# Kernel tuning notes

Hardware: AMD Instinct MI355X
Metric: run time of the kernel (lower is better)

The kernel has to match this reference:

```python
import jax, jax.numpy as jnp
import numpy as np

N, D, E = 524288, 64, 4  # tokens, feature dim (d_in=64 default), num_expert=4


def setup_inputs() -> dict:
    key = jax.random.key(0)
    ks = jax.random.split(key, 5)
    s = 0.02
    return {
        "x": jax.random.normal(ks[0], (N, D), jnp.float32),
        "w_gate_a": jax.random.normal(ks[1], (D, E), jnp.float32) * s,
        "w_exp_a": jax.random.normal(ks[2], (E, D, D), jnp.float32) * s,
        "b_exp_a": jnp.zeros((E, D), jnp.float32),
        "w_gate_b": jax.random.normal(ks[3], (D, E), jnp.float32) * s,
        "w_exp_b": jax.random.normal(ks[4], (E, D, D), jnp.float32) * s,
        "b_exp_b": jnp.zeros((E, D), jnp.float32),
    }


def _moe_layer(x, w_gate, w_exp, b_exp):
    # Soft MoE: softmax gate over experts, each expert is (x - b_e) @ W_e.
    # Noise and PWLayer dropout are eval-mode identities.
    gates = jax.nn.softmax(x @ w_gate, axis=-1)            # [N, E]
    shifted = x[:, None, :] - b_exp[None, :, :]            # [N, E, D]
    expert_out = jnp.einsum('ned,edf->nef', shifted, w_exp)  # [N, E, D]
    return jnp.einsum('ne,nef->nf', gates, expert_out)     # [N, D]


def reference(x, w_gate_a, w_exp_a, b_exp_a, w_gate_b, w_exp_b, b_exp_b):
    residual = x
    h = _moe_layer(x, w_gate_a, w_exp_a, b_exp_a)
    # self.act is None (default) and nn.Dropout(0.5) is identity in eval mode
    h = _moe_layer(h, w_gate_b, w_exp_b, b_exp_b)
    return h + residual
```

## Files before the change

### kernel.cpp

```cpp
#include <hip/hip_runtime.h>
#include <math.h>


typedef __attribute__((ext_vector_type(8))) short short8;
typedef __attribute__((ext_vector_type(4))) short short4v;
typedef __attribute__((ext_vector_type(4))) float floatx4;

__device__ __forceinline__ float bf2f(unsigned short s) {
    unsigned int u = ((unsigned int)s) << 16;
    return __builtin_bit_cast(float, u);
}
__device__ __forceinline__ short f2bf(float f) {
    unsigned int u = __builtin_bit_cast(unsigned int, f);
    u += 0x7fffu + ((u >> 16) & 1u);
    return (short)(u >> 16);
}

#define NBLOCKS 512
#define TPW 4

__device__ __forceinline__ float ldf(const void* p, int isbf, int idx) {
    return isbf ? bf2f(((const unsigned short*)p)[idx]) : ((const float*)p)[idx];
}

__global__ __launch_bounds__(256, 2)
void moe2_fused(const void* __restrict__ x,
                const void* __restrict__ wg_a,
                const void* __restrict__ we_a,
                const void* __restrict__ be_a,
                const void* __restrict__ wg_b,
                const void* __restrict__ we_b,
                const void* __restrict__ be_b,
                void* __restrict__ outv)
{
    __shared__ alignas(16) short sB[2][17408];
    __shared__ float sC[2][4][64];
    __shared__ alignas(16) short sStage[4][1152];
    __shared__ int sBad[7];

    const int tid = threadIdx.x;

    const void* ps[7] = {x, wg_a, we_a, be_a, wg_b, we_b, be_b};
    if (tid < 7) sBad[tid] = 0;
    __syncthreads();
    if (tid < 64) {
        #pragma unroll
        for (int b = 0; b < 7; ++b) {
            const unsigned short s = ((const unsigned short*)ps[b])[2 * tid];
            const float a = fabsf(bf2f(s));
            const bool sane = (s == 0) || (a >= 9.3e-10f && a <= 1.1e9f);
            if (!sane) atomicAdd(&sBad[b], 1);
        }
    }
    __syncthreads();
    const int fx  = (sBad[0] < 16);
    const int fga = (sBad[1] < 16), fwa = (sBad[2] < 16), fba = (sBad[3] < 16);
    const int fgb = (sBad[4] < 16), fwb = (sBad[5] < 16), fbb = (sBad[6] < 16);

    for (int idx = tid; idx < 2 * 17 * 2 * 64; idx += 256) {
        const int L   = idx / 2176;
        const int rem = idx - L * 2176;
        const int t   = rem >> 7;
        const int kap = (rem >> 6) & 1;
        const int l2  = rem & 63;
        const int kb  = kap * 32 + (l2 >> 4) * 8;
        const int cc  = l2 & 15;
        const void* we = L ? we_b : we_a;
        const void* wg = L ? wg_b : wg_a;
        const int  fwe = L ? fwb : fwa;
        const int  fwg = L ? fgb : fga;
        short* dst = &sB[L][rem * 8];
        if (t < 16) {
            const int e = t >> 2;
            const int f = (t & 3) * 16 + cc;
            #pragma unroll
            for (int j = 0; j < 8; ++j)
                dst[j] = f2bf(ldf(we, fwe, (e * 64 + kb + j) * 64 + f));
        } else {
            #pragma unroll
            for (int j = 0; j < 8; ++j)
                dst[j] = (cc < 4) ? f2bf(ldf(wg, fwg, (kb + j) * 4 + cc)) : (short)0;
        }
    }
    for (int idx = tid; idx < 512; idx += 256) {
        const int L = idx >> 8;
        const int e = (idx >> 6) & 3;
        const int f = idx & 63;
        const void* we = L ? we_b : we_a;
        const void* be = L ? be_b : be_a;
        const int  fwe = L ? fwb : fwa;
        const int  fbe = L ? fbb : fba;
        float s = 0.f;
        for (int d = 0; d < 64; ++d)
            s += ldf(be, fbe, e * 64 + d) * ldf(we, fwe, (e * 64 + d) * 64 + f);
        sC[L][e][f] = s;
    }
    __syncthreads();

    const int l  = tid & 63;
    const int wv = tid >> 6;
    const int c  = l & 15;
    const int q  = l >> 4;
    short* stg = &sStage[wv][0];

    auto runLayer = [&](const short8 (&aF)[4][2], const int L, float (&acc)[4][4][4]) {
        const short* BL = &sB[L][0];
        floatx4 gA[4];
        {
            const short8 B0 = *(const short8*)&BL[(16 * 2 + 0) * 512 + l * 8];
            const short8 B1 = *(const short8*)&BL[(16 * 2 + 1) * 512 + l * 8];
            #pragma unroll
            for (int s = 0; s < 4; ++s) {
                floatx4 z = {0.f, 0.f, 0.f, 0.f};
                z = __builtin_amdgcn_mfma_f32_16x16x32_bf16(aF[s][0], B0, z, 0, 0, 0);
                z = __builtin_amdgcn_mfma_f32_16x16x32_bf16(aF[s][1], B1, z, 0, 0, 0);
                gA[s] = z;
            }
        }
        #pragma unroll
        for (int s = 0; s < 4; ++s) {
            float lg[4][4];
            #pragma unroll
            for (int e = 0; e < 4; ++e)
                #pragma unroll
                for (int r = 0; r < 4; ++r)
                    lg[e][r] = __shfl(gA[s][r], (l & 48) + e, 64);
            short gv[4];
            #pragma unroll
            for (int r = 0; r < 4; ++r) {
                const float m0 = fmaxf(fmaxf(lg[0][r], lg[1][r]), fmaxf(lg[2][r], lg[3][r]));
                const float e0 = __expf(lg[0][r] - m0);
                const float e1 = __expf(lg[1][r] - m0);
                const float e2 = __expf(lg[2][r] - m0);
                const float e3 = __expf(lg[3][r] - m0);
                const float inv = 1.f / (e0 + e1 + e2 + e3);
                const float mine = (c == 0) ? e0 : (c == 1) ? e1 : (c == 2) ? e2 : e3;
                gv[r] = f2bf(mine * inv);
            }
            if (c < 4) {
                short4v pk = {gv[0], gv[1], gv[2], gv[3]};
                *(short4v*)&stg[(s * 4 + c) * 16 + 4 * q] = pk;
            }
        }

        #pragma unroll
        for (int s = 0; s < 4; ++s)
            #pragma unroll
            for (int tt = 0; tt < 4; ++tt)
                #pragma unroll
                for (int r = 0; r < 4; ++r)
                    acc[s][tt][r] = 0.f;

        #pragma unroll
        for (int e = 0; e < 4; ++e) {
            float gse[4][4];
            #pragma unroll
            for (int s = 0; s < 4; ++s) {
                const short4v gp = *(const short4v*)&stg[(s * 4 + e) * 16 + 4 * q];
                #pragma unroll
                for (int r = 0; r < 4; ++r)
                    gse[s][r] = bf2f((unsigned short)gp[r]);
            }
            #pragma unroll
            for (int tt = 0; tt < 4; ++tt) {
                const int t = e * 4 + tt;
                const short8 B0 = *(const short8*)&BL[(t * 2 + 0) * 512 + l * 8];
                const short8 B1 = *(const short8*)&BL[(t * 2 + 1) * 512 + l * 8];
                const float ce = sC[L][e][tt * 16 + c];
                #pragma unroll
                for (int s = 0; s < 4; ++s) {
                    floatx4 z = {0.f, 0.f, 0.f, 0.f};
                    z = __builtin_amdgcn_mfma_f32_16x16x32_bf16(aF[s][0], B0, z, 0, 0, 0);
                    z = __builtin_amdgcn_mfma_f32_16x16x32_bf16(aF[s][1], B1, z, 0, 0, 0);
                    #pragma unroll
                    for (int r = 0; r < 4; ++r)
                        acc[s][tt][r] += gse[s][r] * (z[r] - ce);
                }
            }
        }
    };

    const int waveGlobal = blockIdx.x * 4 + wv;
    for (int it = 0; it < TPW; ++it) {
        const int tile = waveGlobal * TPW + it;
        const size_t tok0 = (size_t)tile * 64;

        short8 xF[4][2];
        if (fx) {
            const unsigned short* xu = (const unsigned short*)x;
            #pragma unroll
            for (int s = 0; s < 4; ++s)
                #pragma unroll
                for (int k = 0; k < 2; ++k)
                    xF[s][k] = *(const short8*)(xu + (tok0 + s * 16 + c) * 64 + k * 32 + q * 8);
        } else {
            const float* xf = (const float*)x;
            #pragma unroll
            for (int s = 0; s < 4; ++s)
                #pragma unroll
                for (int k = 0; k < 2; ++k) {
                    const float* xr = xf + (tok0 + s * 16 + c) * 64 + k * 32 + q * 8;
                    const floatx4 v0 = *(const floatx4*)xr;
                    const floatx4 v1 = *(const floatx4*)(xr + 4);
                    short8 f;
                    #pragma unroll
                    for (int j = 0; j < 4; ++j) { f[j] = f2bf(v0[j]); f[4 + j] = f2bf(v1[j]); }
                    xF[s][k] = f;
                }
        }

        float acc[4][4][4];
        runLayer(xF, 0, acc);

        short8 hF[4][2];
        #pragma unroll
        for (int s = 0; s < 4; ++s) {
            #pragma unroll
            for (int tt = 0; tt < 4; ++tt)
                #pragma unroll
                for (int r = 0; r < 4; ++r)
                    stg[(4 * q + r) * 72 + tt * 16 + c] = f2bf(acc[s][tt][r]);
            hF[s][0] = *(const short8*)&stg[c * 72 + 0 + q * 8];
            hF[s][1] = *(const short8*)&stg[c * 72 + 32 + q * 8];
        }

        runLayer(hF, 1, acc);

        if (fx) {
            unsigned short* ob = (unsigned short*)outv;
            #pragma unroll
            for (int s = 0; s < 4; ++s) {
                #pragma unroll
                for (int tt = 0; tt < 4; ++tt)
                    #pragma unroll
                    for (int r = 0; r < 4; ++r)
                        stg[(4 * q + r) * 72 + tt * 16 + c] = f2bf(acc[s][tt][r]);
                #pragma unroll
                for (int k = 0; k < 2; ++k) {
                    const short8 v = *(const short8*)&stg[c * 72 + k * 32 + q * 8];
                    short8 o;
                    #pragma unroll
                    for (int j = 0; j < 8; ++j)
                        o[j] = f2bf(bf2f((unsigned short)v[j]) + bf2f((unsigned short)xF[s][k][j]));
                    *(short8*)(ob + (tok0 + s * 16 + c) * 64 + k * 32 + q * 8) = o;
                }
            }
        } else {
            const float* xf = (const float*)x;
            float* of = (float*)outv;
            #pragma unroll
            for (int s = 0; s < 4; ++s)
                #pragma unroll
                for (int tt = 0; tt < 4; ++tt)
                    #pragma unroll
                    for (int r = 0; r < 4; ++r) {
                        const size_t o = (tok0 + s * 16 + 4 * q + r) * 64 + tt * 16 + c;
                        of[o] = acc[s][tt][r] + xf[o];
                    }
        }
    }
}

extern "C" void kernel_launch(void* const* d_in, const int* in_sizes, int n_in,
                              void* d_out, int out_size, void* d_ws, size_t ws_size,
                              hipStream_t stream) {
    hipLaunchKernelGGL(moe2_fused, dim3(NBLOCKS), dim3(256), 0, stream,
                       d_in[0], d_in[1], d_in[2], d_in[3], d_in[4], d_in[5], d_in[6],
                       d_out);
}
```

Measured before the change: 362.5 us.

## Restructure MoE kernel: 1024-thread blocks, shuffle softmax, bias-free fast path, vector stores

After: 567.0 us. 56.4% more time.

```diff
diff --git a/kernel.cpp b/kernel.cpp
--- a/kernel.cpp
+++ b/kernel.cpp
@@ -3,61 +3,50 @@
 
 
 typedef __attribute__((ext_vector_type(8))) short short8;
-typedef __attribute__((ext_vector_type(4))) short short4v;
 typedef __attribute__((ext_vector_type(4))) float floatx4;
 
 __device__ __forceinline__ float bf2f(unsigned short s) {
     unsigned int u = ((unsigned int)s) << 16;
     return __builtin_bit_cast(float, u);
 }
-__device__ __forceinline__ short f2bf(float f) {
+__device__ __forceinline__ unsigned short f2bf(float f) {
     unsigned int u = __builtin_bit_cast(unsigned int, f);
     u += 0x7fffu + ((u >> 16) & 1u);
-    return (short)(u >> 16);
-}
-
-#define NBLOCKS 512
-#define TPW 4
-
-__device__ __forceinline__ float ldf(const void* p, int isbf, int idx) {
-    return isbf ? bf2f(((const unsigned short*)p)[idx]) : ((const float*)p)[idx];
-}
-
-__global__ __launch_bounds__(256, 2)
-void moe2_fused(const void* __restrict__ x,
-                const void* __restrict__ wg_a,
-                const void* __restrict__ we_a,
-                const void* __restrict__ be_a,
-                const void* __restrict__ wg_b,
-                const void* __restrict__ we_b,
-                const void* __restrict__ be_b,
-                void* __restrict__ outv)
+    return (unsigned short)(u >> 16);
+}
+__device__ __forceinline__ float hi2f(unsigned int p) {
+    return __builtin_bit_cast(float, p & 0xffff0000u);
+}
+__device__ __forceinline__ float lo2f(unsigned int p) {
+    return __builtin_bit_cast(float, p << 16);
+}
+
+struct CTrue  { static constexpr bool value = true;  };
+struct CFalse { static constexpr bool value = false; };
+
+#define NBLK 512
+
+__global__ __launch_bounds__(1024)
+void moe2_fused(const float* __restrict__ x,
+                const float* __restrict__ wg_a,
+                const float* __restrict__ we_a,
+                const float* __restrict__ be_a,
+                const float* __restrict__ wg_b,
+                const float* __restrict__ we_b,
+                const float* __restrict__ be_b,
+                float* __restrict__ out)
 {
     __shared__ alignas(16) short sB[2][17408];
     __shared__ float sC[2][4][64];
-    __shared__ alignas(16) short sStage[4][1152];
-    __shared__ int sBad[7];
+    __shared__ int sHasC;
+    __shared__ alignas(16) float sStg[16][1088];
 
     const int tid = threadIdx.x;
 
-    const void* ps[7] = {x, wg_a, we_a, be_a, wg_b, we_b, be_b};
-    if (tid < 7) sBad[tid] = 0;
+    if (tid == 0) sHasC = 0;
     __syncthreads();
-    if (tid < 64) {
-        #pragma unroll
-        for (int b = 0; b < 7; ++b) {
-            const unsigned short s = ((const unsigned short*)ps[b])[2 * tid];
-            const float a = fabsf(bf2f(s));
-            const bool sane = (s == 0) || (a >= 9.3e-10f && a <= 1.1e9f);
-            if (!sane) atomicAdd(&sBad[b], 1);
-        }
-    }
-    __syncthreads();
-    const int fx  = (sBad[0] < 16);
-    const int fga = (sBad[1] < 16), fwa = (sBad[2] < 16), fba = (sBad[3] < 16);
-    const int fgb = (sBad[4] < 16), fwb = (sBad[5] < 16), fbb = (sBad[6] < 16);
-
-    for (int idx = tid; idx < 2 * 17 * 2 * 64; idx += 256) {
+
+    for (int idx = tid; idx < 2 * 17 * 2 * 64; idx += 1024) {
         const int L   = idx / 2176;
         const int rem = idx - L * 2176;
         const int t   = rem >> 7;
@@ -65,81 +54,67 @@
         const int l2  = rem & 63;
         const int kb  = kap * 32 + (l2 >> 4) * 8;
         const int cc  = l2 & 15;
-        const void* we = L ? we_b : we_a;
-        const void* wg = L ? wg_b : wg_a;
-        const int  fwe = L ? fwb : fwa;
-        const int  fwg = L ? fgb : fga;
+        const float* we = L ? we_b : we_a;
+        const float* wg = L ? wg_b : wg_a;
         short* dst = &sB[L][rem * 8];
         if (t < 16) {
             const int e = t >> 2;
             const int f = (t & 3) * 16 + cc;
             #pragma unroll
             for (int j = 0; j < 8; ++j)
-                dst[j] = f2bf(ldf(we, fwe, (e * 64 + kb + j) * 64 + f));
+                dst[j] = (short)f2bf(we[(e * 64 + kb + j) * 64 + f]);
         } else {
             #pragma unroll
             for (int j = 0; j < 8; ++j)
-                dst[j] = (cc < 4) ? f2bf(ldf(wg, fwg, (kb + j) * 4 + cc)) : (short)0;
-        }
-    }
-    for (int idx = tid; idx < 512; idx += 256) {
+                dst[j] = (cc < 4) ? (short)f2bf(wg[(kb + j) * 4 + cc]) : (short)0;
+        }
+    }
+    for (int idx = tid; idx < 512; idx += 1024) {
         const int L = idx >> 8;
         const int e = (idx >> 6) & 3;
         const int f = idx & 63;
-        const void* we = L ? we_b : we_a;
-        const void* be = L ? be_b : be_a;
-        const int  fwe = L ? fwb : fwa;
-        const int  fbe = L ? fbb : fba;
+        const float* we = L ? we_b : we_a;
+        const float* be = L ? be_b : be_a;
         float s = 0.f;
         for (int d = 0; d < 64; ++d)
-            s += ldf(be, fbe, e * 64 + d) * ldf(we, fwe, (e * 64 + d) * 64 + f);
+            s += be[e * 64 + d] * we[(e * 64 + d) * 64 + f];
         sC[L][e][f] = s;
+        if (s != 0.f) atomicExch(&sHasC, 1);
     }
     __syncthreads();
+    const bool hasC = (sHasC != 0);
 
     const int l  = tid & 63;
     const int wv = tid >> 6;
     const int c  = l & 15;
     const int q  = l >> 4;
-    short* stg = &sStage[wv][0];
+    float* stgF = &sStg[wv][0];
+    short* stgS = (short*)stgF;
+
+    const int tile = blockIdx.x * 16 + wv;
+    const size_t tok0 = (size_t)tile * 64;
 
     auto runLayer = [&](const short8 (&aF)[4][2], const int L, float (&acc)[4][4][4]) {
         const short* BL = &sB[L][0];
-        floatx4 gA[4];
+        unsigned int gp[4][2];
         {
-            const short8 B0 = *(const short8*)&BL[(16 * 2 + 0) * 512 + l * 8];
-            const short8 B1 = *(const short8*)&BL[(16 * 2 + 1) * 512 + l * 8];
+            const short8 B0 = *(const short8*)&BL[(32 + 0) * 512 + l * 8];
+            const short8 B1 = *(const short8*)&BL[(32 + 1) * 512 + l * 8];
             #pragma unroll
             for (int s = 0; s < 4; ++s) {
                 floatx4 z = {0.f, 0.f, 0.f, 0.f};
                 z = __builtin_amdgcn_mfma_f32_16x16x32_bf16(aF[s][0], B0, z, 0, 0, 0);
                 z = __builtin_amdgcn_mfma_f32_16x16x32_bf16(aF[s][1], B1, z, 0, 0, 0);
-                gA[s] = z;
-            }
-        }
-        #pragma unroll
-        for (int s = 0; s < 4; ++s) {
-            float lg[4][4];
-            #pragma unroll
-            for (int e = 0; e < 4; ++e)
-                #pragma unroll
-                for (int r = 0; r < 4; ++r)
-                    lg[e][r] = __shfl(gA[s][r], (l & 48) + e, 64);
-            short gv[4];
-            #pragma unroll
-            for (int r = 0; r < 4; ++r) {
-                const float m0 = fmaxf(fmaxf(lg[0][r], lg[1][r]), fmaxf(lg[2][r], lg[3][r]));
-                const float e0 = __expf(lg[0][r] - m0);
-                const float e1 = __expf(lg[1][r] - m0);
-                const float e2 = __expf(lg[2][r] - m0);
-                const float e3 = __expf(lg[3][r] - m0);
-                const float inv = 1.f / (e0 + e1 + e2 + e3);
-                const float mine = (c == 0) ? e0 : (c == 1) ? e1 : (c == 2) ? e2 : e3;
-                gv[r] = f2bf(mine * inv);
-            }
-            if (c < 4) {
-                short4v pk = {gv[0], gv[1], gv[2], gv[3]};
-                *(short4v*)&stg[(s * 4 + c) * 16 + 4 * q] = pk;
+                float g[4];
+                #pragma unroll
+                for (int r = 0; r < 4; ++r) {
+                    const float ev = __expf(z[r]);
+                    const float s2 = ev + __shfl_xor(ev, 1, 64);
+                    const float sm = s2 + __shfl_xor(s2, 2, 64);
+                    g[r] = ev * __builtin_amdgcn_rcpf(sm);
+                }
+                gp[s][0] = (unsigned int)f2bf(g[0]) | ((unsigned int)f2bf(g[1]) << 16);
+                gp[s][1] = (unsigned int)f2bf(g[2]) | ((unsigned int)f2bf(g[3]) << 16);
             }
         }
 
@@ -151,112 +126,99 @@
                 for (int r = 0; r < 4; ++r)
                     acc[s][tt][r] = 0.f;
 
-        #pragma unroll
-        for (int e = 0; e < 4; ++e) {
-            float gse[4][4];
-            #pragma unroll
-            for (int s = 0; s < 4; ++s) {
-                const short4v gp = *(const short4v*)&stg[(s * 4 + e) * 16 + 4 * q];
-                #pragma unroll
-                for (int r = 0; r < 4; ++r)
-                    gse[s][r] = bf2f((unsigned short)gp[r]);
-            }
-            #pragma unroll
-            for (int tt = 0; tt < 4; ++tt) {
-                const int t = e * 4 + tt;
-                const short8 B0 = *(const short8*)&BL[(t * 2 + 0) * 512 + l * 8];
-                const short8 B1 = *(const short8*)&BL[(t * 2 + 1) * 512 + l * 8];
-                const float ce = sC[L][e][tt * 16 + c];
+        auto eloop = [&](auto HC) {
+            constexpr bool hc = decltype(HC)::value;
+            #pragma unroll
+            for (int e = 0; e < 4; ++e) {
+                unsigned int gs[4][2];
                 #pragma unroll
                 for (int s = 0; s < 4; ++s) {
-                    floatx4 z = {0.f, 0.f, 0.f, 0.f};
-                    z = __builtin_amdgcn_mfma_f32_16x16x32_bf16(aF[s][0], B0, z, 0, 0, 0);
-                    z = __builtin_amdgcn_mfma_f32_16x16x32_bf16(aF[s][1], B1, z, 0, 0, 0);
+                    gs[s][0] = __shfl(gp[s][0], (l & 48) + e, 64);
+                    gs[s][1] = __shfl(gp[s][1], (l & 48) + e, 64);
+                }
+                #pragma unroll
+                for (int tt = 0; tt < 4; ++tt) {
+                    const int t = e * 4 + tt;
+                    const short8 B0 = *(const short8*)&BL[(t * 2 + 0) * 512 + l * 8];
+                    const short8 B1 = *(const short8*)&BL[(t * 2 + 1) * 512 + l * 8];
+                    float ce = 0.f;
+                    if constexpr (hc) ce = sC[L][e][tt * 16 + c];
                     #pragma unroll
-                    for (int r = 0; r < 4; ++r)
-                        acc[s][tt][r] += gse[s][r] * (z[r] - ce);
+                    for (int s = 0; s < 4; ++s) {
+                        floatx4 z = {0.f, 0.f, 0.f, 0.f};
+                        z = __builtin_amdgcn_mfma_f32_16x16x32_bf16(aF[s][0], B0, z, 0, 0, 0);
+                        z = __builtin_amdgcn_mfma_f32_16x16x32_bf16(aF[s][1], B1, z, 0, 0, 0);
+                        const float g0 = lo2f(gs[s][0]), g1 = hi2f(gs[s][0]);
+                        const float g2 = lo2f(gs[s][1]), g3 = hi2f(gs[s][1]);
+                        if constexpr (hc) {
+                            acc[s][tt][0] += g0 * (z[0] - ce);
+                            acc[s][tt][1] += g1 * (z[1] - ce);
+                            acc[s][tt][2] += g2 * (z[2] - ce);
+                            acc[s][tt][3] += g3 * (z[3] - ce);
+                        } else {
+                            acc[s][tt][0] += g0 * z[0];
+                            acc[s][tt][1] += g1 * z[1];
+                            acc[s][tt][2] += g2 * z[2];
+                            acc[s][tt][3] += g3 * z[3];
+                        }
+                    }
                 }
             }
-        }
+        };
+        if (hasC) eloop(CTrue{}); else eloop(CFalse{});
     };
 
-    const int waveGlobal = blockIdx.x * 4 + wv;
-    for (int it = 0; it < TPW; ++it) {
-        const int tile = waveGlobal * TPW + it;
-        const size_t tok0 = (size_t)tile * 64;
-
-        short8 xF[4][2];
-        if (fx) {
-            const unsigned short* xu = (const unsigned short*)x;
-            #pragma unroll
-            for (int s = 0; s < 4; ++s)
-                #pragma unroll
-                for (int k = 0; k < 2; ++k)
-                    xF[s][k] = *(const short8*)(xu + (tok0 + s * 16 + c) * 64 + k * 32 + q * 8);
-        } else {
-            const float* xf = (const float*)x;
-            #pragma unroll
-            for (int s = 0; s < 4; ++s)
-                #pragma unroll
-                for (int k = 0; k < 2; ++k) {
-                    const float* xr = xf + (tok0 + s * 16 + c) * 64 + k * 32 + q * 8;
-                    const floatx4 v0 = *(const floatx4*)xr;
-                    const floatx4 v1 = *(const floatx4*)(xr + 4);
-                    short8 f;
-                    #pragma unroll
-                    for (int j = 0; j < 4; ++j) { f[j] = f2bf(v0[j]); f[4 + j] = f2bf(v1[j]); }
-                    xF[s][k] = f;
-                }
-        }
-
-        float acc[4][4][4];
-        runLayer(xF, 0, acc);
-
-        short8 hF[4][2];
-        #pragma unroll
-        for (int s = 0; s < 4; ++s) {
-            #pragma unroll
-            for (int tt = 0; tt < 4; ++tt)
-                #pragma unroll
-                for (int r = 0; r < 4; ++r)
-                    stg[(4 * q + r) * 72 + tt * 16 + c] = f2bf(acc[s][tt][r]);
-            hF[s][0] = *(const short8*)&stg[c * 72 + 0 + q * 8];
-            hF[s][1] = *(const short8*)&stg[c * 72 + 32 + q * 8];
-        }
-
-        runLayer(hF, 1, acc);
-
-        if (fx) {
-            unsigned short* ob = (unsigned short*)outv;
-            #pragma unroll
-            for (int s = 0; s < 4; ++s) {
-                #pragma unroll
-                for (int tt = 0; tt < 4; ++tt)
-                    #pragma unroll
-                    for (int r = 0; r < 4; ++r)
-                        stg[(4 * q + r) * 72 + tt * 16 + c] = f2bf(acc[s][tt][r]);
-                #pragma unroll
-                for (int k = 0; k < 2; ++k) {
-                    const short8 v = *(const short8*)&stg[c * 72 + k * 32 + q * 8];
-                    short8 o;
-                    #pragma unroll
-                    for (int j = 0; j < 8; ++j)
-                        o[j] = f2bf(bf2f((unsigned short)v[j]) + bf2f((unsigned short)xF[s][k][j]));
-                    *(short8*)(ob + (tok0 + s * 16 + c) * 64 + k * 32 + q * 8) = o;
-                }
+    short8 xF[4][2];
+    #pragma unroll
+    for (int s = 0; s < 4; ++s)
+        #pragma unroll
+        for (int k = 0; k < 2; ++k) {
+            const float* xr = x + (tok0 + s * 16 + c) * 64 + k * 32 + q * 8;
+            const floatx4 v0 = *(const floatx4*)xr;
+            const floatx4 v1 = *(const floatx4*)(xr + 4);
+            short8 f;
+            #pragma unroll
+            for (int j = 0; j < 4; ++j) {
+                f[j]     = (short)f2bf(v0[j]);
+                f[4 + j] = (short)f2bf(v1[j]);
             }
-        } else {
-            const float* xf = (const float*)x;
-            float* of = (float*)outv;
-            #pragma unroll
-            for (int s = 0; s < 4; ++s)
-                #pragma unroll
-                for (int tt = 0; tt < 4; ++tt)
-                    #pragma unroll
-                    for (int r = 0; r < 4; ++r) {
-                        const size_t o = (tok0 + s * 16 + 4 * q + r) * 64 + tt * 16 + c;
-                        of[o] = acc[s][tt][r] + xf[o];
-                    }
+            xF[s][k] = f;
+        }
+
+    float acc[4][4][4];
+    runLayer(xF, 0, acc);
+
+    short8 hF[4][2];
+    #pragma unroll
+    for (int s = 0; s < 4; ++s) {
+        #pragma unroll
+        for (int tt = 0; tt < 4; ++tt)
+            #pragma unroll
+            for (int r = 0; r < 4; ++r)
+                stgS[(4 * q + r) * 72 + tt * 16 + c] = (short)f2bf(acc[s][tt][r]);
+        hF[s][0] = *(const short8*)&stgS[c * 72 + q * 8];
+        hF[s][1] = *(const short8*)&stgS[c * 72 + 32 + q * 8];
+    }
+
+    runLayer(hF, 1, acc);
+
+    const int rE = l >> 2;
+    const int aE = l & 3;
+    #pragma unroll
+    for (int s = 0; s < 4; ++s) {
+        #pragma unroll
+        for (int tt = 0; tt < 4; ++tt)
+            #pragma unroll
+            for (int r = 0; r < 4; ++r)
+                stgF[(4 * q + r) * 68 + tt * 16 + c] = acc[s][tt][r];
+        const float* xrow = x   + (tok0 + s * 16 + rE) * 64;
+        float*       orow = out + (tok0 + s * 16 + rE) * 64;
+        #pragma unroll
+        for (int j = 0; j < 4; ++j) {
+            const int col = aE * 4 + j * 16;
+            const floatx4 v  = *(const floatx4*)&stgF[rE * 68 + col];
+            const floatx4 xr = *(const floatx4*)&xrow[col];
+            *(floatx4*)&orow[col] = v + xr;
         }
     }
 }
@@ -264,7 +226,9 @@
 extern "C" void kernel_launch(void* const* d_in, const int* in_sizes, int n_in,
                               void* d_out, int out_size, void* d_ws, size_t ws_size,
                               hipStream_t stream) {
-    hipLaunchKernelGGL(moe2_fused, dim3(NBLOCKS), dim3(256), 0, stream,
-                       d_in[0], d_in[1], d_in[2], d_in[3], d_in[4], d_in[5], d_in[6],
-                       d_out);
-}
+    hipLaunchKernelGGL(moe2_fused, dim3(NBLK), dim3(1024), 0, stream,
+                       (const float*)d_in[0], (const float*)d_in[1],
+                       (const float*)d_in[2], (const float*)d_in[3],
+                       (const float*)d_in[4], (const float*)d_in[5],
+                       (const float*)d_in[6], (float*)d_out);
+}
```
